# Performance work log

Hardware: AMD Instinct MI355X
Metric: run time of the kernel (lower is better)

The kernel has to match this reference:

```python
import jax, jax.numpy as jnp
import numpy as np

N_AGENTS = 8
N_ACTIONS = 14
STATE_DIM = 168
RNN_DIM = 64
GAT_DIM = 32
N_HEADS = 4
HYPER = 64


def setup_inputs() -> dict:
    key = jax.random.key(0)
    ks = jax.random.split(key, 16)
    bs, T = 256, 256
    def xavier(k, shape):
        fan_in, fan_out = shape[0], shape[-1]
        lim = float(np.sqrt(6.0 / (fan_in + fan_out)))
        return jax.random.uniform(k, shape, jnp.float32, -lim, lim)
    return {
        'agent_qs': jax.random.normal(ks[0], (bs, T, N_AGENTS), jnp.float32),
        'states': jax.random.normal(ks[1], (bs, T, STATE_DIM), jnp.float32),
        'max_q_i': jax.random.normal(ks[2], (bs, T, N_AGENTS), jnp.float32),
        'hidden_states': jax.random.normal(ks[3], (bs, T, N_AGENTS, RNN_DIM), jnp.float32),
        # hyper_w_final MLP
        'w1f': xavier(ks[4], (STATE_DIM, HYPER)), 'b1f': jnp.zeros((HYPER,), jnp.float32),
        'w2f': xavier(ks[5], (HYPER, N_AGENTS)), 'b2f': jnp.zeros((N_AGENTS,), jnp.float32),
        # V MLP
        'w1v': xavier(ks[6], (STATE_DIM, HYPER)), 'b1v': jnp.zeros((HYPER,), jnp.float32),
        'w2v': xavier(ks[7], (HYPER, N_AGENTS)), 'b2v': jnp.zeros((N_AGENTS,), jnp.float32),
        # GAT: W (no bias) and attention vector att_a [1, H, 2*d]
        'Wg': xavier(ks[8], (RNN_DIM, N_HEADS * GAT_DIM)),
        'att_a': xavier(ks[9], (1, N_HEADS, 2 * GAT_DIM)) * 1.414,
        # hyper_w_dvd linear
        'Wd': xavier(ks[10], (STATE_DIM, N_HEADS * GAT_DIM)), 'bd': jnp.zeros((N_HEADS * GAT_DIM,), jnp.float32),
    }


def reference(agent_qs, states, max_q_i, hidden_states,
              w1f, b1f, w2f, b2f, w1v, b1v, w2v, b2v,
              Wg, att_a, Wd, bd):
    bs = agent_qs.shape[0]
    S = states.reshape(-1, STATE_DIM)                     # [B, state_dim]
    q = agent_qs.reshape(-1, N_AGENTS)                    # [B, n]
    mq = max_q_i.reshape(-1, N_AGENTS)
    H = hidden_states.reshape(-1, N_AGENTS, RNN_DIM)      # [B, n, rnn]

    # weighted_head=True branch
    w_final = jnp.abs(jax.nn.relu(S @ w1f + b1f) @ w2f + b2f) + 1e-10
    v = jax.nn.relu(S @ w1v + b1v) @ w2v + b2v
    q = w_final * q + v
    mq = w_final * mq + v
    adv_q = jax.lax.stop_gradient(q - mq)                 # .detach() in torch

    # MultiHeadGAT on tiny agent graph, without materializing h_cat
    hp = jnp.einsum('bni,ihd->bhnd', H, Wg.reshape(RNN_DIM, N_HEADS, GAT_DIM))  # [B,h,n,d]
    a_i = att_a[0, :, :GAT_DIM]                           # [h, d]
    a_j = att_a[0, :, GAT_DIM:]
    e_i = jnp.einsum('bhnd,hd->bhn', hp, a_i)
    e_j = jnp.einsum('bhnd,hd->bhn', hp, a_j)
    e = e_i[:, :, :, None] + e_j[:, :, None, :]           # [B,h,n,n]
    e = jnp.where(e > 0, e, 0.2 * e)                      # LeakyReLU(0.2)
    attn = jax.nn.softmax(e, axis=-1)
    graphs = jax.nn.elu(jnp.einsum('bhij,bhjd->bhid', attn, hp))  # [B,h,n,d]

    # DVD weights
    w_dvd = (S @ Wd + bd).reshape(-1, N_HEADS, GAT_DIM)   # [B,h,d]
    weights_dvd = jnp.abs(jnp.einsum('bhd,bhnd->bhn', w_dvd, graphs))  # [B,h,n]
    adv_w_final = weights_dvd.mean(axis=1)                # [B,n]

    # is_minus_one=True
    adv_tot = jnp.sum(adv_q * (adv_w_final - 1.0), axis=1)
    return adv_tot.reshape(bs, -1, 1)
```

## Files before the change

kernel.cpp:

```cpp
#include <hip/hip_runtime.h>
#include <math.h>

#define STATE_DIM 168
#define BTOT 65536
#define SLS 1064
#define SPAD 184

typedef float f32x4 __attribute__((ext_vector_type(4)));
typedef short bf16x8 __attribute__((ext_vector_type(8)));

union Frag { bf16x8 v; unsigned short u[8]; };
union Acc  { f32x4 v; float f[4]; };

__device__ __forceinline__ unsigned short f2bf(float f) {
    unsigned int u = __float_as_uint(f);
    u += 0x7fffu + ((u >> 16) & 1u);
    return (unsigned short)(u >> 16);
}

__global__ void __launch_bounds__(256)
ffn_kernel(const float* __restrict__ states,
           const float* __restrict__ w1f, const float* __restrict__ b1f,
           const float* __restrict__ w2f, const float* __restrict__ b2f,
           const float* __restrict__ Wd,  const float* __restrict__ bd,
           float* __restrict__ wfin, float* __restrict__ wdvd)
{
    __shared__ unsigned short S_bf[16 * SPAD];
    __shared__ float y1[16 * 72];

    const int t    = threadIdx.x;
    const int wid  = t >> 6;
    const int lane = t & 63;
    const int quad = lane >> 4;
    const int col  = lane & 15;

    Frag B[3][6];
    #pragma unroll
    for (int ks = 0; ks < 6; ++ks)
        #pragma unroll
        for (int j = 0; j < 8; ++j) {
            const int k = ks * 32 + quad * 8 + j;
            const bool v = (k < STATE_DIM);
            B[0][ks].u[j] = v ? f2bf(w1f[k * 64 + wid * 16 + col]) : (unsigned short)0;
            B[1][ks].u[j] = v ? f2bf(Wd[k * 128 + wid * 32 + col]) : (unsigned short)0;
            B[2][ks].u[j] = v ? f2bf(Wd[k * 128 + wid * 32 + 16 + col]) : (unsigned short)0;
        }
    Frag B2[2];
    #pragma unroll
    for (int ks = 0; ks < 2; ++ks)
        #pragma unroll
        for (int j = 0; j < 8; ++j) {
            const int k = ks * 32 + quad * 8 + j;
            B2[ks].u[j] = (col < 8) ? f2bf(w2f[k * 8 + col]) : (unsigned short)0;
        }

    const float bias1  = b1f[wid * 16 + col];
    const float biasd0 = bd[wid * 32 + col];
    const float biasd1 = bd[wid * 32 + 16 + col];
    const float bias2  = (col < 8) ? b2f[col] : 0.0f;

    for (int it = 0; it < 2; ++it) {
        const long smp0 = ((long)blockIdx.x * 2 + it) * 16;

        {
            const int r = t >> 4, u = t & 15;
            const float* Srow = states + (smp0 + r) * STATE_DIM;
            #pragma unroll
            for (int i = 0; i < 12; ++i) {
                const int k = u + 16 * i;
                if (k < SPAD) {
                    unsigned short vv = (k < STATE_DIM) ? f2bf(Srow[k])
                                                        : (unsigned short)0;
                    S_bf[r * SPAD + k] = vv;
                }
            }
        }
        __syncthreads();

        Frag A[6];
        #pragma unroll
        for (int ks = 0; ks < 6; ++ks) {
            int k0 = ks * 32 + quad * 8;
            if (ks == 5 && quad != 0) k0 = STATE_DIM;
            A[ks].v = *(const bf16x8*)&S_bf[col * SPAD + k0];
        }

        Acc D0, D1, D2t;
        D0.v = (f32x4){0.f,0.f,0.f,0.f};
        D1.v = (f32x4){0.f,0.f,0.f,0.f};
        D2t.v = (f32x4){0.f,0.f,0.f,0.f};
        #pragma unroll
        for (int ks = 0; ks < 6; ++ks) {
            D0.v  = __builtin_amdgcn_mfma_f32_16x16x32_bf16(A[ks].v, B[0][ks].v, D0.v, 0, 0, 0);
            D1.v  = __builtin_amdgcn_mfma_f32_16x16x32_bf16(A[ks].v, B[1][ks].v, D1.v, 0, 0, 0);
            D2t.v = __builtin_amdgcn_mfma_f32_16x16x32_bf16(A[ks].v, B[2][ks].v, D2t.v, 0, 0, 0);
        }

        #pragma unroll
        for (int r = 0; r < 4; ++r) {
            const int m = quad * 4 + r;
            y1[m * 72 + wid * 16 + col] = fmaxf(D0.f[r] + bias1, 0.0f);
            wdvd[(smp0 + m) * 128 + wid * 32 + col]      = D1.f[r]  + biasd0;
            wdvd[(smp0 + m) * 128 + wid * 32 + 16 + col] = D2t.f[r] + biasd1;
        }
        __syncthreads();

        {
            Frag A2[2];
            #pragma unroll
            for (int ks = 0; ks < 2; ++ks) {
                const float4 p0 = *(const float4*)&y1[col * 72 + ks * 32 + quad * 8];
                const float4 p1 = *(const float4*)&y1[col * 72 + ks * 32 + quad * 8 + 4];
                A2[ks].u[0] = f2bf(p0.x); A2[ks].u[1] = f2bf(p0.y);
                A2[ks].u[2] = f2bf(p0.z); A2[ks].u[3] = f2bf(p0.w);
                A2[ks].u[4] = f2bf(p1.x); A2[ks].u[5] = f2bf(p1.y);
                A2[ks].u[6] = f2bf(p1.z); A2[ks].u[7] = f2bf(p1.w);
            }
            Acc Dw;
            Dw.v = (f32x4){0.f,0.f,0.f,0.f};
            Dw.v = __builtin_amdgcn_mfma_f32_16x16x32_bf16(A2[0].v, B2[0].v, Dw.v, 0, 0, 0);
            Dw.v = __builtin_amdgcn_mfma_f32_16x16x32_bf16(A2[1].v, B2[1].v, Dw.v, 0, 0, 0);
            if (wid == 0 && col < 8) {
                #pragma unroll
                for (int r = 0; r < 4; ++r)
                    wfin[(smp0 + quad * 4 + r) * 8 + col] =
                        fabsf(Dw.f[r] + bias2) + 1e-10f;
            }
        }
        __syncthreads();
    }
}

__global__ void __launch_bounds__(256, 3)
gat_kernel(const float* __restrict__ agent_qs,
           const float* __restrict__ max_q_i,
           const float* __restrict__ hidden,
           const float* __restrict__ Wg,
           const float* __restrict__ att_a,
           const float* __restrict__ wfin,
           const float* __restrict__ wdvd,
           float* __restrict__ out)
{
    __shared__ float hp_lds[4][2 * SLS];
    __shared__ float attn_lds[4][544];
    __shared__ float e_lds[4][128];
    __shared__ float ws_lds[4][64];
    __shared__ float a_lds[264];

    const int t    = threadIdx.x;
    const int wid  = t >> 6;
    const int lane = t & 63;

    {
        const int h = t >> 6, r = t & 63, wch = r >> 5, d = r & 31;
        a_lds[(h * 2 + wch) * 33 + d] = att_a[t];
    }
    __syncthreads();

    float* hp  = hp_lds[wid];
    float* at  = attn_lds[wid];
    float* el  = e_lds[wid];
    float* wsl = ws_lds[wid];

    const int wgid = blockIdx.x * 4 + wid;
    const int quad = lane >> 4;
    const int col  = lane & 15;

    Frag Bf[8][2];
    #pragma unroll
    for (int tt = 0; tt < 8; ++tt)
        #pragma unroll
        for (int ks = 0; ks < 2; ++ks)
            #pragma unroll
            for (int j = 0; j < 8; ++j)
                Bf[tt][ks].u[j] =
                    f2bf(Wg[(ks * 32 + quad * 8 + j) * 128 + tt * 16 + col]);

    const int sl_a = (lane >> 3) & 1;
    const int n_a  = lane & 7;
    const int sl_w = quad >> 1;
    const int nb   = (quad & 1) * 4;

    for (int g = 0; g < 4; ++g) {
        const long smp0 = (long)wgid * 8 + 2 * g;

        Frag A0, A1;
        {
            const float* Hb = hidden + (smp0 + sl_a) * 512 + n_a * 64 + quad * 8;
            const float4 h00 = *(const float4*)(Hb);
            const float4 h01 = *(const float4*)(Hb + 4);
            const float4 h10 = *(const float4*)(Hb + 32);
            const float4 h11 = *(const float4*)(Hb + 36);
            A0.u[0] = f2bf(h00.x); A0.u[1] = f2bf(h00.y);
            A0.u[2] = f2bf(h00.z); A0.u[3] = f2bf(h00.w);
            A0.u[4] = f2bf(h01.x); A0.u[5] = f2bf(h01.y);
            A0.u[6] = f2bf(h01.z); A0.u[7] = f2bf(h01.w);
            A1.u[0] = f2bf(h10.x); A1.u[1] = f2bf(h10.y);
            A1.u[2] = f2bf(h10.z); A1.u[3] = f2bf(h10.w);
            A1.u[4] = f2bf(h11.x); A1.u[5] = f2bf(h11.y);
            A1.u[6] = f2bf(h11.z); A1.u[7] = f2bf(h11.w);
        }

        #pragma unroll
        for (int tt = 0; tt < 8; ++tt) {
            Acc acc;
            acc.v = (f32x4){0.f, 0.f, 0.f, 0.f};
            acc.v = __builtin_amdgcn_mfma_f32_16x16x32_bf16(A0.v, Bf[tt][0].v, acc.v, 0, 0, 0);
            acc.v = __builtin_amdgcn_mfma_f32_16x16x32_bf16(A1.v, Bf[tt][1].v, acc.v, 0, 0, 0);
            const int c = tt * 16 + col;
            float4 st = {acc.f[0], acc.f[1], acc.f[2], acc.f[3]};
            *(float4*)&hp[sl_w * SLS + c * 8 + ((c >> 5) << 3) + nb] = st;
        }

        {
            const int h = lane >> 4, r = lane & 15, wch = r >> 3, n = r & 7;
            const float* arow = &a_lds[(h * 2 + wch) * 33];
            #pragma unroll
            for (int sl = 0; sl < 2; ++sl) {
                float acc = 0.f;
                #pragma unroll
                for (int d = 0; d < 32; ++d)
                    acc = fmaf(hp[sl * SLS + (h * 32 + d) * 8 + h * 8 + n],
                               arow[d], acc);
                el[sl * 64 + wch * 32 + h * 8 + n] = acc;
            }
        }

        {
            const int sl = lane >> 5, r = lane & 31, h = r >> 3, i = r & 7;
            const float eiv = el[sl * 64 + h * 8 + i];
            const float* ejp = &el[sl * 64 + 32 + h * 8];
            float e[8], mx = -1e30f;
            #pragma unroll
            for (int j = 0; j < 8; ++j) {
                float v = eiv + ejp[j];
                v = v > 0.f ? v : 0.2f * v;
                e[j] = v;
                mx = fmaxf(mx, v);
            }
            float ssum = 0.f;
            #pragma unroll
            for (int j = 0; j < 8; ++j) { e[j] = __expf(e[j] - mx); ssum += e[j]; }
            const float inv = 1.f / ssum;
            #pragma unroll
            for (int j = 0; j < 8; ++j)
                at[sl * 272 + h * 66 + i * 8 + j] = e[j] * inv;
        }

        {
            const int sl = lane >> 5, r = lane & 31, h = r >> 3, n = r & 7;
            const long smp = smp0 + sl;
            float ar[8];
            #pragma unroll
            for (int j = 0; j < 8; ++j)
                ar[j] = at[sl * 272 + h * 66 + n * 8 + j];
            float wdd[32];
            {
                const float* wdp = wdvd + smp * 128 + h * 32;
                #pragma unroll
                for (int q4 = 0; q4 < 8; ++q4) {
                    const float4 v = *(const float4*)(wdp + q4 * 4);
                    wdd[q4 * 4 + 0] = v.x; wdd[q4 * 4 + 1] = v.y;
                    wdd[q4 * 4 + 2] = v.z; wdd[q4 * 4 + 3] = v.w;
                }
            }
            float part = 0.f;
            #pragma unroll
            for (int d = 0; d < 32; ++d) {
                const int c = h * 32 + d;
                const float* hb = &hp[sl * SLS + c * 8 + h * 8];
                const float4 p0 = *(const float4*)(hb);
                const float4 p1 = *(const float4*)(hb + 4);
                float gg = ar[0] * p0.x;
                gg = fmaf(ar[1], p0.y, gg);
                gg = fmaf(ar[2], p0.z, gg);
                gg = fmaf(ar[3], p0.w, gg);
                gg = fmaf(ar[4], p1.x, gg);
                gg = fmaf(ar[5], p1.y, gg);
                gg = fmaf(ar[6], p1.z, gg);
                gg = fmaf(ar[7], p1.w, gg);
                gg = gg > 0.f ? gg : (__expf(gg) - 1.0f);
                part = fmaf(wdd[d], gg, part);
            }
            wsl[sl * 32 + h * 8 + n] = fabsf(part);
        }

        {
            const int sl = lane >> 5, r = lane & 31;
            if (r < 8) {
                const int n = r;
                const long smp = smp0 + sl;
                const float awf = 0.25f * (wsl[sl * 32 + n] + wsl[sl * 32 + 8 + n] +
                                           wsl[sl * 32 + 16 + n] + wsl[sl * 32 + 24 + n]);
                const float adv = wfin[smp * 8 + n] *
                                  (agent_qs[smp * 8 + n] - max_q_i[smp * 8 + n]);
                float p = adv * (awf - 1.0f);
                p += __shfl_xor(p, 4, 64);
                p += __shfl_xor(p, 2, 64);
                p += __shfl_xor(p, 1, 64);
                if (n == 0) out[smp] = p;
            }
        }
    }
}

extern "C" void kernel_launch(void* const* d_in, const int* in_sizes, int n_in,
                              void* d_out, int out_size, void* d_ws, size_t ws_size,
                              hipStream_t stream) {
    const float* agent_qs = (const float*)d_in[0];
    const float* states   = (const float*)d_in[1];
    const float* max_q_i  = (const float*)d_in[2];
    const float* hidden   = (const float*)d_in[3];
    const float* w1f = (const float*)d_in[4];
    const float* b1f = (const float*)d_in[5];
    const float* w2f = (const float*)d_in[6];
    const float* b2f = (const float*)d_in[7];
    const float* Wg    = (const float*)d_in[12];
    const float* att_a = (const float*)d_in[13];
    const float* Wd    = (const float*)d_in[14];
    const float* bd    = (const float*)d_in[15];
    float* out  = (float*)d_out;

    float* wfin = (float*)d_ws;
    float* wdvd = wfin + (size_t)BTOT * 8;

    ffn_kernel<<<2048, 256, 0, stream>>>(states, w1f, b1f, w2f, b2f, Wd, bd,
                                         wfin, wdvd);
    gat_kernel<<<2048, 256, 0, stream>>>(agent_qs, max_q_i, hidden, Wg, att_a,
                                         wfin, wdvd, out);
}
```

Baseline: 331.3 us.

## Fuse hypernet FFN and GAT kernels, keeping intermediate weights in LDS

Merges the state-MLP kernel and the GAT kernel into one launch. Each block computes w_final and w_dvd for its 32 samples into shared memory, then runs the GAT stage on the same samples. This removes the global-memory write and reread of the per-sample DVD weights and w_final, plus one kernel launch. In exchange, LDS use per block grows and occupancy drops to 2 blocks per CU, which may reduce latency hiding for the hidden-state loads.

```diff
diff --git a/kernel.cpp b/kernel.cpp
--- a/kernel.cpp
+++ b/kernel.cpp
@@ -18,287 +18,282 @@
     return (unsigned short)(u >> 16);
 }
 
-__global__ void __launch_bounds__(256)
-ffn_kernel(const float* __restrict__ states,
-           const float* __restrict__ w1f, const float* __restrict__ b1f,
-           const float* __restrict__ w2f, const float* __restrict__ b2f,
-           const float* __restrict__ Wd,  const float* __restrict__ bd,
-           float* __restrict__ wfin, float* __restrict__ wdvd)
-{
-    __shared__ unsigned short S_bf[16 * SPAD];
-    __shared__ float y1[16 * 72];
-
-    const int t    = threadIdx.x;
-    const int wid  = t >> 6;
-    const int lane = t & 63;
-    const int quad = lane >> 4;
-    const int col  = lane & 15;
-
-    Frag B[3][6];
-    #pragma unroll
-    for (int ks = 0; ks < 6; ++ks)
-        #pragma unroll
-        for (int j = 0; j < 8; ++j) {
-            const int k = ks * 32 + quad * 8 + j;
-            const bool v = (k < STATE_DIM);
-            B[0][ks].u[j] = v ? f2bf(w1f[k * 64 + wid * 16 + col]) : (unsigned short)0;
-            B[1][ks].u[j] = v ? f2bf(Wd[k * 128 + wid * 32 + col]) : (unsigned short)0;
-            B[2][ks].u[j] = v ? f2bf(Wd[k * 128 + wid * 32 + 16 + col]) : (unsigned short)0;
-        }
-    Frag B2[2];
-    #pragma unroll
-    for (int ks = 0; ks < 2; ++ks)
-        #pragma unroll
-        for (int j = 0; j < 8; ++j) {
-            const int k = ks * 32 + quad * 8 + j;
-            B2[ks].u[j] = (col < 8) ? f2bf(w2f[k * 8 + col]) : (unsigned short)0;
-        }
-
-    const float bias1  = b1f[wid * 16 + col];
-    const float biasd0 = bd[wid * 32 + col];
-    const float biasd1 = bd[wid * 32 + 16 + col];
-    const float bias2  = (col < 8) ? b2f[col] : 0.0f;
-
-    for (int it = 0; it < 2; ++it) {
-        const long smp0 = ((long)blockIdx.x * 2 + it) * 16;
-
-        {
-            const int r = t >> 4, u = t & 15;
-            const float* Srow = states + (smp0 + r) * STATE_DIM;
-            #pragma unroll
-            for (int i = 0; i < 12; ++i) {
-                const int k = u + 16 * i;
-                if (k < SPAD) {
-                    unsigned short vv = (k < STATE_DIM) ? f2bf(Srow[k])
-                                                        : (unsigned short)0;
-                    S_bf[r * SPAD + k] = vv;
-                }
-            }
-        }
-        __syncthreads();
-
-        Frag A[6];
-        #pragma unroll
-        for (int ks = 0; ks < 6; ++ks) {
-            int k0 = ks * 32 + quad * 8;
-            if (ks == 5 && quad != 0) k0 = STATE_DIM;
-            A[ks].v = *(const bf16x8*)&S_bf[col * SPAD + k0];
-        }
-
-        Acc D0, D1, D2t;
-        D0.v = (f32x4){0.f,0.f,0.f,0.f};
-        D1.v = (f32x4){0.f,0.f,0.f,0.f};
-        D2t.v = (f32x4){0.f,0.f,0.f,0.f};
-        #pragma unroll
-        for (int ks = 0; ks < 6; ++ks) {
-            D0.v  = __builtin_amdgcn_mfma_f32_16x16x32_bf16(A[ks].v, B[0][ks].v, D0.v, 0, 0, 0);
-            D1.v  = __builtin_amdgcn_mfma_f32_16x16x32_bf16(A[ks].v, B[1][ks].v, D1.v, 0, 0, 0);
-            D2t.v = __builtin_amdgcn_mfma_f32_16x16x32_bf16(A[ks].v, B[2][ks].v, D2t.v, 0, 0, 0);
-        }
-
-        #pragma unroll
-        for (int r = 0; r < 4; ++r) {
-            const int m = quad * 4 + r;
-            y1[m * 72 + wid * 16 + col] = fmaxf(D0.f[r] + bias1, 0.0f);
-            wdvd[(smp0 + m) * 128 + wid * 32 + col]      = D1.f[r]  + biasd0;
-            wdvd[(smp0 + m) * 128 + wid * 32 + 16 + col] = D2t.f[r] + biasd1;
-        }
-        __syncthreads();
-
-        {
-            Frag A2[2];
-            #pragma unroll
-            for (int ks = 0; ks < 2; ++ks) {
-                const float4 p0 = *(const float4*)&y1[col * 72 + ks * 32 + quad * 8];
-                const float4 p1 = *(const float4*)&y1[col * 72 + ks * 32 + quad * 8 + 4];
-                A2[ks].u[0] = f2bf(p0.x); A2[ks].u[1] = f2bf(p0.y);
-                A2[ks].u[2] = f2bf(p0.z); A2[ks].u[3] = f2bf(p0.w);
-                A2[ks].u[4] = f2bf(p1.x); A2[ks].u[5] = f2bf(p1.y);
-                A2[ks].u[6] = f2bf(p1.z); A2[ks].u[7] = f2bf(p1.w);
-            }
-            Acc Dw;
-            Dw.v = (f32x4){0.f,0.f,0.f,0.f};
-            Dw.v = __builtin_amdgcn_mfma_f32_16x16x32_bf16(A2[0].v, B2[0].v, Dw.v, 0, 0, 0);
-            Dw.v = __builtin_amdgcn_mfma_f32_16x16x32_bf16(A2[1].v, B2[1].v, Dw.v, 0, 0, 0);
-            if (wid == 0 && col < 8) {
-                #pragma unroll
-                for (int r = 0; r < 4; ++r)
-                    wfin[(smp0 + quad * 4 + r) * 8 + col] =
-                        fabsf(Dw.f[r] + bias2) + 1e-10f;
-            }
-        }
-        __syncthreads();
-    }
-}
-
-__global__ void __launch_bounds__(256, 3)
-gat_kernel(const float* __restrict__ agent_qs,
-           const float* __restrict__ max_q_i,
-           const float* __restrict__ hidden,
-           const float* __restrict__ Wg,
-           const float* __restrict__ att_a,
-           const float* __restrict__ wfin,
-           const float* __restrict__ wdvd,
-           float* __restrict__ out)
+__global__ void __launch_bounds__(256, 2)
+fused_kernel(const float* __restrict__ states,
+             const float* __restrict__ w1f, const float* __restrict__ b1f,
+             const float* __restrict__ w2f, const float* __restrict__ b2f,
+             const float* __restrict__ Wd,  const float* __restrict__ bd,
+             const float* __restrict__ agent_qs,
+             const float* __restrict__ max_q_i,
+             const float* __restrict__ hidden,
+             const float* __restrict__ Wg,
+             const float* __restrict__ att_a,
+             float* __restrict__ out)
 {
     __shared__ float hp_lds[4][2 * SLS];
     __shared__ float attn_lds[4][544];
     __shared__ float e_lds[4][128];
     __shared__ float ws_lds[4][64];
     __shared__ float a_lds[264];
+    __shared__ float wdvd_lds[32 * 144];
+    __shared__ float wfin_lds[32 * 8];
+
+    unsigned short* S_bf = (unsigned short*)&hp_lds[0][0];
+    float*          y1   = &hp_lds[2][0];
 
     const int t    = threadIdx.x;
     const int wid  = t >> 6;
     const int lane = t & 63;
+    const int quad = lane >> 4;
+    const int col  = lane & 15;
 
     {
         const int h = t >> 6, r = t & 63, wch = r >> 5, d = r & 31;
         a_lds[(h * 2 + wch) * 33 + d] = att_a[t];
     }
-    __syncthreads();
-
-    float* hp  = hp_lds[wid];
-    float* at  = attn_lds[wid];
-    float* el  = e_lds[wid];
-    float* wsl = ws_lds[wid];
-
-    const int wgid = blockIdx.x * 4 + wid;
-    const int quad = lane >> 4;
-    const int col  = lane & 15;
-
-    Frag Bf[8][2];
-    #pragma unroll
-    for (int tt = 0; tt < 8; ++tt)
+
+    const long blk0 = (long)blockIdx.x * 32;
+
+    {
+        Frag B[3][6];
+        #pragma unroll
+        for (int ks = 0; ks < 6; ++ks)
+            #pragma unroll
+            for (int j = 0; j < 8; ++j) {
+                const int k = ks * 32 + quad * 8 + j;
+                const bool v = (k < STATE_DIM);
+                B[0][ks].u[j] = v ? f2bf(w1f[k * 64 + wid * 16 + col]) : (unsigned short)0;
+                B[1][ks].u[j] = v ? f2bf(Wd[k * 128 + wid * 32 + col]) : (unsigned short)0;
+                B[2][ks].u[j] = v ? f2bf(Wd[k * 128 + wid * 32 + 16 + col]) : (unsigned short)0;
+            }
+        Frag B2[2];
         #pragma unroll
         for (int ks = 0; ks < 2; ++ks)
             #pragma unroll
-            for (int j = 0; j < 8; ++j)
-                Bf[tt][ks].u[j] =
-                    f2bf(Wg[(ks * 32 + quad * 8 + j) * 128 + tt * 16 + col]);
-
-    const int sl_a = (lane >> 3) & 1;
-    const int n_a  = lane & 7;
-    const int sl_w = quad >> 1;
-    const int nb   = (quad & 1) * 4;
-
-    for (int g = 0; g < 4; ++g) {
-        const long smp0 = (long)wgid * 8 + 2 * g;
-
-        Frag A0, A1;
-        {
-            const float* Hb = hidden + (smp0 + sl_a) * 512 + n_a * 64 + quad * 8;
-            const float4 h00 = *(const float4*)(Hb);
-            const float4 h01 = *(const float4*)(Hb + 4);
-            const float4 h10 = *(const float4*)(Hb + 32);
-            const float4 h11 = *(const float4*)(Hb + 36);
-            A0.u[0] = f2bf(h00.x); A0.u[1] = f2bf(h00.y);
-            A0.u[2] = f2bf(h00.z); A0.u[3] = f2bf(h00.w);
-            A0.u[4] = f2bf(h01.x); A0.u[5] = f2bf(h01.y);
-            A0.u[6] = f2bf(h01.z); A0.u[7] = f2bf(h01.w);
-            A1.u[0] = f2bf(h10.x); A1.u[1] = f2bf(h10.y);
-            A1.u[2] = f2bf(h10.z); A1.u[3] = f2bf(h10.w);
-            A1.u[4] = f2bf(h11.x); A1.u[5] = f2bf(h11.y);
-            A1.u[6] = f2bf(h11.z); A1.u[7] = f2bf(h11.w);
+            for (int j = 0; j < 8; ++j) {
+                const int k = ks * 32 + quad * 8 + j;
+                B2[ks].u[j] = (col < 8) ? f2bf(w2f[k * 8 + col]) : (unsigned short)0;
+            }
+
+        const float bias1  = b1f[wid * 16 + col];
+        const float biasd0 = bd[wid * 32 + col];
+        const float biasd1 = bd[wid * 32 + 16 + col];
+        const float bias2  = (col < 8) ? b2f[col] : 0.0f;
+
+        for (int it = 0; it < 2; ++it) {
+            const long smp0 = blk0 + it * 16;
+
+            {
+                const int r = t >> 4, u = t & 15;
+                const float* Srow = states + (smp0 + r) * STATE_DIM;
+                #pragma unroll
+                for (int i = 0; i < 12; ++i) {
+                    const int k = u + 16 * i;
+                    if (k < SPAD) {
+                        unsigned short vv = (k < STATE_DIM) ? f2bf(Srow[k])
+                                                            : (unsigned short)0;
+                        S_bf[r * SPAD + k] = vv;
+                    }
+                }
+            }
+            __syncthreads();
+
+            Frag A[6];
+            #pragma unroll
+            for (int ks = 0; ks < 6; ++ks) {
+                int k0 = ks * 32 + quad * 8;
+                if (ks == 5 && quad != 0) k0 = STATE_DIM;
+                A[ks].v = *(const bf16x8*)&S_bf[col * SPAD + k0];
+            }
+
+            Acc D0, D1, D2t;
+            D0.v = (f32x4){0.f,0.f,0.f,0.f};
+            D1.v = (f32x4){0.f,0.f,0.f,0.f};
+            D2t.v = (f32x4){0.f,0.f,0.f,0.f};
+            #pragma unroll
+            for (int ks = 0; ks < 6; ++ks) {
+                D0.v  = __builtin_amdgcn_mfma_f32_16x16x32_bf16(A[ks].v, B[0][ks].v, D0.v, 0, 0, 0);
+                D1.v  = __builtin_amdgcn_mfma_f32_16x16x32_bf16(A[ks].v, B[1][ks].v, D1.v, 0, 0, 0);
+                D2t.v = __builtin_amdgcn_mfma_f32_16x16x32_bf16(A[ks].v, B[2][ks].v, D2t.v, 0, 0, 0);
+            }
+
+            #pragma unroll
+            for (int r = 0; r < 4; ++r) {
+                const int m = quad * 4 + r;
+                const int l = it * 16 + m;
+                y1[m * 72 + wid * 16 + col] = fmaxf(D0.f[r] + bias1, 0.0f);
+                wdvd_lds[l * 144 + wid * 36 + col]      = D1.f[r]  + biasd0;
+                wdvd_lds[l * 144 + wid * 36 + 16 + col] = D2t.f[r] + biasd1;
+            }
+            __syncthreads();
+
+            {
+                Frag A2[2];
+                #pragma unroll
+                for (int ks = 0; ks < 2; ++ks) {
+                    const float4 p0 = *(const float4*)&y1[col * 72 + ks * 32 + quad * 8];
+                    const float4 p1 = *(const float4*)&y1[col * 72 + ks * 32 + quad * 8 + 4];
+                    A2[ks].u[0] = f2bf(p0.x); A2[ks].u[1] = f2bf(p0.y);
+                    A2[ks].u[2] = f2bf(p0.z); A2[ks].u[3] = f2bf(p0.w);
+                    A2[ks].u[4] = f2bf(p1.x); A2[ks].u[5] = f2bf(p1.y);
+                    A2[ks].u[6] = f2bf(p1.z); A2[ks].u[7] = f2bf(p1.w);
+                }
+                Acc Dw;
+                Dw.v = (f32x4){0.f,0.f,0.f,0.f};
+                Dw.v = __builtin_amdgcn_mfma_f32_16x16x32_bf16(A2[0].v, B2[0].v, Dw.v, 0, 0, 0);
+                Dw.v = __builtin_amdgcn_mfma_f32_16x16x32_bf16(A2[1].v, B2[1].v, Dw.v, 0, 0, 0);
+                if (wid == 0 && col < 8) {
+                    #pragma unroll
+                    for (int r = 0; r < 4; ++r)
+                        wfin_lds[(it * 16 + quad * 4 + r) * 8 + col] =
+                            fabsf(Dw.f[r] + bias2) + 1e-10f;
+                }
+            }
+            __syncthreads();
         }
-
+    }
+
+    {
+        float* hp  = hp_lds[wid];
+        float* at  = attn_lds[wid];
+        float* el  = e_lds[wid];
+        float* wsl = ws_lds[wid];
+
+        Frag Bf[8][2];
         #pragma unroll
-        for (int tt = 0; tt < 8; ++tt) {
-            Acc acc;
-            acc.v = (f32x4){0.f, 0.f, 0.f, 0.f};
-            acc.v = __builtin_amdgcn_mfma_f32_16x16x32_bf16(A0.v, Bf[tt][0].v, acc.v, 0, 0, 0);
-            acc.v = __builtin_amdgcn_mfma_f32_16x16x32_bf16(A1.v, Bf[tt][1].v, acc.v, 0, 0, 0);
-            const int c = tt * 16 + col;
-            float4 st = {acc.f[0], acc.f[1], acc.f[2], acc.f[3]};
-            *(float4*)&hp[sl_w * SLS + c * 8 + ((c >> 5) << 3) + nb] = st;
-        }
-
-        {
-            const int h = lane >> 4, r = lane & 15, wch = r >> 3, n = r & 7;
-            const float* arow = &a_lds[(h * 2 + wch) * 33];
-            #pragma unroll
-            for (int sl = 0; sl < 2; ++sl) {
-                float acc = 0.f;
-                #pragma unroll
-                for (int d = 0; d < 32; ++d)
-                    acc = fmaf(hp[sl * SLS + (h * 32 + d) * 8 + h * 8 + n],
-                               arow[d], acc);
-                el[sl * 64 + wch * 32 + h * 8 + n] = acc;
-            }
-        }
-
-        {
-            const int sl = lane >> 5, r = lane & 31, h = r >> 3, i = r & 7;
-            const float eiv = el[sl * 64 + h * 8 + i];
-            const float* ejp = &el[sl * 64 + 32 + h * 8];
-            float e[8], mx = -1e30f;
-            #pragma unroll
-            for (int j = 0; j < 8; ++j) {
-                float v = eiv + ejp[j];
-                v = v > 0.f ? v : 0.2f * v;
-                e[j] = v;
-                mx = fmaxf(mx, v);
-            }
-            float ssum = 0.f;
-            #pragma unroll
-            for (int j = 0; j < 8; ++j) { e[j] = __expf(e[j] - mx); ssum += e[j]; }
-            const float inv = 1.f / ssum;
-            #pragma unroll
-            for (int j = 0; j < 8; ++j)
-                at[sl * 272 + h * 66 + i * 8 + j] = e[j] * inv;
-        }
-
-        {
-            const int sl = lane >> 5, r = lane & 31, h = r >> 3, n = r & 7;
-            const long smp = smp0 + sl;
-            float ar[8];
-            #pragma unroll
-            for (int j = 0; j < 8; ++j)
-                ar[j] = at[sl * 272 + h * 66 + n * 8 + j];
-            float wdd[32];
-            {
-                const float* wdp = wdvd + smp * 128 + h * 32;
-                #pragma unroll
-                for (int q4 = 0; q4 < 8; ++q4) {
-                    const float4 v = *(const float4*)(wdp + q4 * 4);
-                    wdd[q4 * 4 + 0] = v.x; wdd[q4 * 4 + 1] = v.y;
-                    wdd[q4 * 4 + 2] = v.z; wdd[q4 * 4 + 3] = v.w;
-                }
-            }
-            float part = 0.f;
-            #pragma unroll
-            for (int d = 0; d < 32; ++d) {
-                const int c = h * 32 + d;
-                const float* hb = &hp[sl * SLS + c * 8 + h * 8];
-                const float4 p0 = *(const float4*)(hb);
-                const float4 p1 = *(const float4*)(hb + 4);
-                float gg = ar[0] * p0.x;
-                gg = fmaf(ar[1], p0.y, gg);
-                gg = fmaf(ar[2], p0.z, gg);
-                gg = fmaf(ar[3], p0.w, gg);
-                gg = fmaf(ar[4], p1.x, gg);
-                gg = fmaf(ar[5], p1.y, gg);
-                gg = fmaf(ar[6], p1.z, gg);
-                gg = fmaf(ar[7], p1.w, gg);
-                gg = gg > 0.f ? gg : (__expf(gg) - 1.0f);
-                part = fmaf(wdd[d], gg, part);
-            }
-            wsl[sl * 32 + h * 8 + n] = fabsf(part);
-        }
-
-        {
-            const int sl = lane >> 5, r = lane & 31;
-            if (r < 8) {
-                const int n = r;
-                const long smp = smp0 + sl;
-                const float awf = 0.25f * (wsl[sl * 32 + n] + wsl[sl * 32 + 8 + n] +
-                                           wsl[sl * 32 + 16 + n] + wsl[sl * 32 + 24 + n]);
-                const float adv = wfin[smp * 8 + n] *
-                                  (agent_qs[smp * 8 + n] - max_q_i[smp * 8 + n]);
-                float p = adv * (awf - 1.0f);
-                p += __shfl_xor(p, 4, 64);
-                p += __shfl_xor(p, 2, 64);
-                p += __shfl_xor(p, 1, 64);
-                if (n == 0) out[smp] = p;
+        for (int tt = 0; tt < 8; ++tt)
+            #pragma unroll
+            for (int ks = 0; ks < 2; ++ks)
+                #pragma unroll
+                for (int j = 0; j < 8; ++j)
+                    Bf[tt][ks].u[j] =
+                        f2bf(Wg[(ks * 32 + quad * 8 + j) * 128 + tt * 16 + col]);
+
+        const int sl_a = (lane >> 3) & 1;
+        const int n_a  = lane & 7;
+        const int sl_w = quad >> 1;
+        const int nb   = (quad & 1) * 4;
+
+        for (int g = 0; g < 4; ++g) {
+            const int  l0   = wid * 8 + 2 * g;
+            const long smp0 = blk0 + l0;
+
+            Frag A0, A1;
+            {
+                const float* Hb = hidden + (smp0 + sl_a) * 512 + n_a * 64 + quad * 8;
+                const float4 h00 = *(const float4*)(Hb);
+                const float4 h01 = *(const float4*)(Hb + 4);
+                const float4 h10 = *(const float4*)(Hb + 32);
+                const float4 h11 = *(const float4*)(Hb + 36);
+                A0.u[0] = f2bf(h00.x); A0.u[1] = f2bf(h00.y);
+                A0.u[2] = f2bf(h00.z); A0.u[3] = f2bf(h00.w);
+                A0.u[4] = f2bf(h01.x); A0.u[5] = f2bf(h01.y);
+                A0.u[6] = f2bf(h01.z); A0.u[7] = f2bf(h01.w);
+                A1.u[0] = f2bf(h10.x); A1.u[1] = f2bf(h10.y);
+                A1.u[2] = f2bf(h10.z); A1.u[3] = f2bf(h10.w);
+                A1.u[4] = f2bf(h11.x); A1.u[5] = f2bf(h11.y);
+                A1.u[6] = f2bf(h11.z); A1.u[7] = f2bf(h11.w);
+            }
+
+            #pragma unroll
+            for (int tt = 0; tt < 8; ++tt) {
+                Acc acc;
+                acc.v = (f32x4){0.f, 0.f, 0.f, 0.f};
+                acc.v = __builtin_amdgcn_mfma_f32_16x16x32_bf16(A0.v, Bf[tt][0].v, acc.v, 0, 0, 0);
+                acc.v = __builtin_amdgcn_mfma_f32_16x16x32_bf16(A1.v, Bf[tt][1].v, acc.v, 0, 0, 0);
+                const int c = tt * 16 + col;
+                float4 st = {acc.f[0], acc.f[1], acc.f[2], acc.f[3]};
+                *(float4*)&hp[sl_w * SLS + c * 8 + ((c >> 5) << 3) + nb] = st;
+            }
+
+            {
+                const int h = lane >> 4, r = lane & 15, wch = r >> 3, n = r & 7;
+                const float* arow = &a_lds[(h * 2 + wch) * 33];
+                #pragma unroll
+                for (int sl = 0; sl < 2; ++sl) {
+                    float acc = 0.f;
+                    #pragma unroll
+                    for (int d = 0; d < 32; ++d)
+                        acc = fmaf(hp[sl * SLS + (h * 32 + d) * 8 + h * 8 + n],
+                                   arow[d], acc);
+                    el[sl * 64 + wch * 32 + h * 8 + n] = acc;
+                }
+            }
+
+            {
+                const int sl = lane >> 5, r = lane & 31, h = r >> 3, i = r & 7;
+                const float eiv = el[sl * 64 + h * 8 + i];
+                const float* ejp = &el[sl * 64 + 32 + h * 8];
+                float e[8], mx = -1e30f;
+                #pragma unroll
+                for (int j = 0; j < 8; ++j) {
+                    float v = eiv + ejp[j];
+                    v = v > 0.f ? v : 0.2f * v;
+                    e[j] = v;
+                    mx = fmaxf(mx, v);
+                }
+                float ssum = 0.f;
+                #pragma unroll
+                for (int j = 0; j < 8; ++j) { e[j] = __expf(e[j] - mx); ssum += e[j]; }
+                const float inv = 1.f / ssum;
+                #pragma unroll
+                for (int j = 0; j < 8; ++j)
+                    at[sl * 272 + h * 66 + i * 8 + j] = e[j] * inv;
+            }
+
+            {
+                const int sl = lane >> 5, r = lane & 31, h = r >> 3, n = r & 7;
+                float ar[8];
+                #pragma unroll
+                for (int j = 0; j < 8; ++j)
+                    ar[j] = at[sl * 272 + h * 66 + n * 8 + j];
+                float wdd[32];
+                {
+                    const float* wdp = &wdvd_lds[(l0 + sl) * 144 + h * 36];
+                    #pragma unroll
+                    for (int q4 = 0; q4 < 8; ++q4) {
+                        const float4 v = *(const float4*)(wdp + q4 * 4);
+                        wdd[q4 * 4 + 0] = v.x; wdd[q4 * 4 + 1] = v.y;
+                        wdd[q4 * 4 + 2] = v.z; wdd[q4 * 4 + 3] = v.w;
+                    }
+                }
+                float part = 0.f;
+                #pragma unroll
+                for (int d = 0; d < 32; ++d) {
+                    const int c = h * 32 + d;
+                    const float* hb = &hp[sl * SLS + c * 8 + h * 8];
+                    const float4 p0 = *(const float4*)(hb);
+                    const float4 p1 = *(const float4*)(hb + 4);
+                    float gg = ar[0] * p0.x;
+                    gg = fmaf(ar[1], p0.y, gg);
+                    gg = fmaf(ar[2], p0.z, gg);
+                    gg = fmaf(ar[3], p0.w, gg);
+                    gg = fmaf(ar[4], p1.x, gg);
+                    gg = fmaf(ar[5], p1.y, gg);
+                    gg = fmaf(ar[6], p1.z, gg);
+                    gg = fmaf(ar[7], p1.w, gg);
+                    gg = gg > 0.f ? gg : (__expf(gg) - 1.0f);
+                    part = fmaf(wdd[d], gg, part);
+                }
+                wsl[sl * 32 + h * 8 + n] = fabsf(part);
+            }
+
+            {
+                const int sl = lane >> 5, r = lane & 31;
+                if (r < 8) {
+                    const int n = r;
+                    const long smp = smp0 + sl;
+                    const int  l   = l0 + sl;
+                    const float awf = 0.25f * (wsl[sl * 32 + n] + wsl[sl * 32 + 8 + n] +
+                                               wsl[sl * 32 + 16 + n] + wsl[sl * 32 + 24 + n]);
+                    const float adv = wfin_lds[l * 8 + n] *
+                                      (agent_qs[smp * 8 + n] - max_q_i[smp * 8 + n]);
+                    float p = adv * (awf - 1.0f);
+                    p += __shfl_xor(p, 4, 64);
+                    p += __shfl_xor(p, 2, 64);
+                    p += __shfl_xor(p, 1, 64);
+                    if (n == 0) out[smp] = p;
+                }
             }
         }
     }
@@ -321,11 +316,9 @@
     const float* bd    = (const float*)d_in[15];
     float* out  = (float*)d_out;
 
-    float* wfin = (float*)d_ws;
-    float* wdvd = wfin + (size_t)BTOT * 8;
-
-    ffn_kernel<<<2048, 256, 0, stream>>>(states, w1f, b1f, w2f, b2f, Wd, bd,
-                                         wfin, wdvd);
-    gat_kernel<<<2048, 256, 0, stream>>>(agent_qs, max_q_i, hidden, Wg, att_a,
-                                         wfin, wdvd, out);
+    (void)d_ws; (void)ws_size;
+
+    fused_kernel<<<2048, 256, 0, stream>>>(states, w1f, b1f, w2f, b2f, Wd, bd,
+                                           agent_qs, max_q_i, hidden, Wg, att_a,
+                                           out);
 }
```

Result: faster. 319.3 us (-3.6%).
